# Kernel optimization log

Measured on AMD Instinct MI355X. Metric: run time of the kernel, lower is better.

The kernel has to match this reference:

```python
import jax, jax.numpy as jnp
import numpy as np

CH = (64, 128, 256, 512)
KV = 960
H = 4          # num_attention_heads; each head owns one channel quarter
EPS = 1e-5     # InstanceNorm2d default eps
B, N = 4, 4096

def _qsplit(x):
    # (B,n,c) -> (B,H,n,c//4): contiguous quarter-split along channels (torch .split)
    b, n, c = x.shape
    return x.reshape(b, n, H, c // H).transpose(0, 2, 1, 3)

def _kvsplit(emb_all):
    # quarter j of emb_all = concat over scales of quarter j of each scale's channel block
    b, n, _ = emb_all.shape
    parts, off = [], 0
    for c in CH:
        parts.append(emb_all[:, :, off:off + c].reshape(b, n, H, c // H))
        off += c
    return jnp.concatenate(parts, axis=-1).transpose(0, 2, 1, 3)  # (B,H,n,240)

def _inorm(s):
    # InstanceNorm2d(H), affine=False: normalize each (b,h) map over its (c,k) extent
    m = jnp.mean(s, axis=(2, 3), keepdims=True)
    v = jnp.var(s, axis=(2, 3), keepdims=True)
    return (s - m) * jax.lax.rsqrt(v + EPS)

def _attend(Q, K, V):
    # Q:(B,H,n,cq)  K,V:(B,H,n,240)  -> (B,n,H*cq)  (channel attention: contract over n)
    scores = jnp.einsum('bhnc,bhnk->bhck', Q, K) / np.float32(np.sqrt(KV))
    probs = jax.nn.softmax(_inorm(scores), axis=-1)
    ctx = jnp.einsum('bhck,bhnk->bnhc', probs, V)
    b, n = ctx.shape[:2]
    return ctx.reshape(b, n, -1)

def setup_inputs() -> dict:
    key = jax.random.key(0)
    ks = iter(jax.random.split(key, 48))
    d = {}
    for name, c in [('emb1', 64), ('emb2', 128), ('emb3', 256), ('emb4', 512)]:
        d[name] = jax.random.normal(next(ks), (B, N, c), jnp.float32)
        d[name.replace('emb', 'embd')] = jax.random.normal(next(ks), (B, N, c), jnp.float32)
    d['emb_all'] = jax.random.normal(next(ks), (B, N, KV), jnp.float32)
    d['emb_alld'] = jax.random.normal(next(ks), (B, N, KV), jnp.float32)
    sc = lambda f: float(1.0 / np.sqrt(f))
    for i, c in enumerate(CH):
        c4 = c // H
        d[f'wq{i+1}'] = jax.random.uniform(next(ks), (H, c4, c4), jnp.float32, -sc(c4), sc(c4))
        d[f'wqd{i+1}'] = jax.random.uniform(next(ks), (H, c4, c4), jnp.float32, -sc(c4), sc(c4))
        d[f'wout{i+1}'] = jax.random.uniform(next(ks), (c, c), jnp.float32, -sc(c), sc(c))
        d[f'woutd{i+1}'] = jax.random.uniform(next(ks), (c, c), jnp.float32, -sc(c), sc(c))
    k4 = KV // H
    for nm in ['wk', 'wv', 'wkd', 'wvd']:  # key/value weights are shared across quarters (module uses index [0])
        d[nm] = jax.random.uniform(next(ks), (k4, k4), jnp.float32, -sc(k4), sc(k4))
    return d

def reference(emb1, emb2, emb3, emb4, emb_all, embd1, embd2, embd3, embd4, emb_alld,
              wq1, wq2, wq3, wq4, wqd1, wqd2, wqd3, wqd4,
              wk, wv, wkd, wvd,
              wout1, wout2, wout3, wout4, woutd1, woutd2, woutd3, woutd4):
    Qs = [jnp.einsum('bhnc,hdc->bhnd', _qsplit(e), w) for e, w in
          zip((emb1, emb2, emb3, emb4), (wq1, wq2, wq3, wq4))]
    Qds = [jnp.einsum('bhnc,hdc->bhnd', _qsplit(e), w) for e, w in
           zip((embd1, embd2, embd3, embd4), (wqd1, wqd2, wqd3, wqd4))]
    kvq, kvqd = _kvsplit(emb_all), _kvsplit(emb_alld)
    K  = jnp.einsum('bhnc,dc->bhnd', kvq,  wk)
    V  = jnp.einsum('bhnc,dc->bhnd', kvq,  wv)
    Kd = jnp.einsum('bhnc,dc->bhnd', kvqd, wkd)
    Vd = jnp.einsum('bhnc,dc->bhnd', kvqd, wvd)
    outs = []
    # cross-modal: optical queries attend to DSM K/V and vice versa
    for Q, w in zip(Qs, (wout1, wout2, wout3, wout4)):
        outs.append(jnp.einsum('bnc,dc->bnd', _attend(Q, Kd, Vd), w))
    for Q, w in zip(Qds, (woutd1, woutd2, woutd3, woutd4)):
        outs.append(jnp.einsum('bnc,dc->bnd', _attend(Q, K, V), w))
    return jnp.concatenate(outs, axis=-1)  # (B, N, 2*960)
```

## Files before the change

### kernel.cpp

```cpp
#include <hip/hip_runtime.h>
#include <hip/hip_bf16.h>

typedef __bf16 bf16_t;
typedef __bf16 bf16x8 __attribute__((ext_vector_type(8)));
typedef float f32x4 __attribute__((ext_vector_type(4)));

static constexpr int B_ = 4, N_ = 4096, H_ = 4;
static constexpr int KS = 40;

__device__ __forceinline__ f32x4 mfma_bf16(bf16x8 a, bf16x8 b, f32x4 c) {
  return __builtin_amdgcn_mfma_f32_16x16x32_bf16(a, b, c, 0, 0, 0);
}

__device__ __forceinline__ void stpk4(bf16_t* d, float4 v) {
  bf16_t t[4] = {(bf16_t)v.x, (bf16_t)v.y, (bf16_t)v.z, (bf16_t)v.w};
  *(uint2*)d = *(const uint2*)t;
}
__device__ __forceinline__ void stz8(bf16_t* d) { *(uint2*)d = make_uint2(0u, 0u); }

__device__ __forceinline__ int kvg(int h, int c) {
  if (c < 16)  return h * 16 + c;
  if (c < 48)  return 64 + h * 32 + c - 16;
  if (c < 112) return 192 + h * 64 + c - 48;
  return 448 + h * 128 + c - 112;
}

__device__ __forceinline__ int qsc(int r) { return (r < 16) ? 0 : (r < 48) ? 1 : (r < 112) ? 2 : 3; }

__global__ __launch_bounds__(256) void k_prep_w(
    const float* __restrict__ wk, const float* __restrict__ wv,
    const float* __restrict__ wkd, const float* __restrict__ wvd,
    const float* __restrict__ wo00, const float* __restrict__ wo01,
    const float* __restrict__ wo02, const float* __restrict__ wo03,
    const float* __restrict__ wo10, const float* __restrict__ wo11,
    const float* __restrict__ wo12, const float* __restrict__ wo13,
    bf16_t* __restrict__ Wkvb, bf16_t* __restrict__ Wob) {
  const float* wkv[4] = {wk, wv, wkd, wvd};
  const float* wo[2][4] = {{wo00, wo01, wo02, wo03}, {wo10, wo11, wo12, wo13}};
  const int soff_f4[5] = {0, 1024, 5120, 21504, 87040};
  for (int i = blockIdx.x * 256 + threadIdx.x; i < 231680; i += gridDim.x * 256) {
    if (i < 57600) {
      int t = i / 14400, r = i - t * 14400;
      float4 v = *(const float4*)(wkv[t] + r * 4);
      stpk4(Wkvb + (size_t)t * 57600 + r * 4, v);
    } else {
      int j = i - 57600;
      int mod = j / 87040, jr = j - mod * 87040;
      int s = (jr < 1024) ? 0 : (jr < 5120) ? 1 : (jr < 21504) ? 2 : 3;
      float4 v = *(const float4*)(wo[mod][s] + (jr - soff_f4[s]) * 4);
      stpk4(Wob + (size_t)mod * 348160 + jr * 4, v);
    }
  }
}

__global__ __launch_bounds__(256) void k_kvsplit(
    const float* __restrict__ eA, const float* __restrict__ eB,
    bf16_t* __restrict__ G) {
  const int TOT = 2 * 16 * 4096 * 30;
  for (int i = blockIdx.x * 256 + threadIdx.x; i < TOT; i += gridDim.x * 256) {
    int t = i / 30;
    int cg = i - t * 30;
    int mod = t >> 16;
    int row = t & 65535;
    int bh = row >> 12, n = row & 4095;
    int b = bh >> 2, h = bh & 3;
    int col = kvg(h, cg * 8);
    const float* src = (mod ? eB : eA) + ((size_t)b * N_ + n) * 960 + col;
    float4 v0 = *(const float4*)src;
    float4 v1 = *(const float4*)(src + 4);
    bf16_t o[8] = {(bf16_t)v0.x, (bf16_t)v0.y, (bf16_t)v0.z, (bf16_t)v0.w,
                   (bf16_t)v1.x, (bf16_t)v1.y, (bf16_t)v1.z, (bf16_t)v1.w};
    *(uint4*)(G + (size_t)t * 240 + cg * 8) = *(const uint4*)o;
  }
}

template <int C4>
__global__ __launch_bounds__(256) void k_proj_q(
    const float* __restrict__ e0, const float* __restrict__ w0, bf16_t* __restrict__ o0,
    const float* __restrict__ e1, const float* __restrict__ w1, bf16_t* __restrict__ o1) {
  constexpr int KP = (C4 < 32) ? 32 : C4;
  constexpr int NF = C4 / 16;
  const float* emb = blockIdx.z ? e1 : e0;
  const float* wq = blockIdx.z ? w1 : w0;
  bf16_t* qout = blockIdx.z ? o1 : o0;
  const int h = blockIdx.y;
  const int m0 = blockIdx.x * 128;
  const int b = m0 >> 12, n0 = m0 & 4095;
  const int tid = threadIdx.x, lane = tid & 63, wid = tid >> 6;
  const int l15 = lane & 15, q = lane >> 4;
  __shared__ bf16_t sA[128 * KS];
  __shared__ bf16_t sB[C4 * KS];
  const f32x4 fz = {0.f, 0.f, 0.f, 0.f};
  f32x4 acc[2][NF];
  for (int i = 0; i < 2; i++) for (int f = 0; f < NF; f++) acc[i][f] = fz;
  const float* srow = emb + ((size_t)b * N_ + n0) * (H_ * C4) + h * C4;
  const float* wb = wq + h * C4 * C4;
  for (int k0 = 0; k0 < KP; k0 += 32) {
    __syncthreads();
    for (int idx = tid; idx < 1024; idx += 256) {
      int r = idx >> 3, cg = idx & 7, c = k0 + cg * 4;
      if (c < C4) stpk4(&sA[r * KS + cg * 4], *(const float4*)(srow + (size_t)r * (H_ * C4) + c));
      else stz8(&sA[r * KS + cg * 4]);
    }
    for (int idx = tid; idx < C4 * 8; idx += 256) {
      int dd = idx >> 3, cg = idx & 7, c = k0 + cg * 4;
      if (c < C4) stpk4(&sB[dd * KS + cg * 4], *(const float4*)(wb + dd * C4 + c));
      else stz8(&sB[dd * KS + cg * 4]);
    }
    __syncthreads();
    const bf16_t* ap = &sA[(wid * 32 + l15) * KS + q * 8];
    bf16x8 a0 = *(const bf16x8*)ap;
    bf16x8 a1 = *(const bf16x8*)(ap + 16 * KS);
    for (int f = 0; f < NF; f++) {
      bf16x8 bb = *(const bf16x8*)&sB[(16 * f + l15) * KS + q * 8];
      acc[0][f] = mfma_bf16(a0, bb, acc[0][f]);
      acc[1][f] = mfma_bf16(a1, bb, acc[1][f]);
    }
  }
  bf16_t* qbh = qout + (size_t)(b * H_ + h) * C4 * 4096;
  for (int i = 0; i < 2; i++)
    for (int f = 0; f < NF; f++) {
      bf16_t pk[4];
      for (int r = 0; r < 4; r++) pk[r] = (bf16_t)acc[i][f][r];
      *(uint2*)(qbh + (size_t)(16 * f + l15) * 4096 + n0 + wid * 32 + 16 * i + q * 4) =
          *(const uint2*)pk;
    }
}

__global__ __launch_bounds__(512) void k_proj_kv(
    const bf16_t* __restrict__ G, const bf16_t* __restrict__ Wkvb,
    bf16_t* __restrict__ Kt0, bf16_t* __restrict__ V0,
    bf16_t* __restrict__ Kt1, bf16_t* __restrict__ V1) {
  const int mod = blockIdx.y;
  const bf16_t* src = G + (size_t)mod * ((size_t)B_ * H_ * N_ * 240);
  const bf16_t* wK = Wkvb + (size_t)(2 * mod) * 57600;
  const bf16_t* wV = Wkvb + (size_t)(2 * mod + 1) * 57600;
  bf16_t* Kt = mod ? Kt1 : Kt0;
  bf16_t* V = mod ? V1 : V0;
  const int m0 = blockIdx.x * 128;
  const int bh = m0 >> 12, n0 = m0 & 4095;
  const int tid = threadIdx.x, lane = tid & 63, wid = tid >> 6;
  const int l15 = lane & 15, q = lane >> 4;
  __shared__ bf16_t sA[128 * KS];
  __shared__ bf16_t sB[2][240 * KS];
  const f32x4 fz = {0.f, 0.f, 0.f, 0.f};
  f32x4 accK[15], accV[15];
  for (int f = 0; f < 15; f++) { accK[f] = fz; accV[f] = fz; }
  const bf16_t* arow = src + (size_t)m0 * 240;
  const uint4 z4 = make_uint4(0u, 0u, 0u, 0u);

  const int ar = tid >> 2, ag = tid & 3;
  int bm[4], bd[4], bg[4];
#pragma unroll
  for (int j = 0; j < 4; j++) {
    int idx = tid + 512 * j;
    bm[j] = idx >= 960;
    int jj = idx - (bm[j] ? 960 : 0);
    bd[j] = jj >> 2; bg[j] = jj & 3;
  }
  uint4 ra, rb0, rb1, rb2, rb3;

#define KV_LOAD(K0)                                                                    \
  {                                                                                    \
    int c = (K0) + ag * 8;                                                             \
    ra = (c < 240) ? *(const uint4*)(arow + (size_t)ar * 240 + c) : z4;                \
    int c0_ = (K0) + bg[0] * 8;                                                        \
    rb0 = (c0_ < 240) ? *(const uint4*)((bm[0] ? wV : wK) + bd[0] * 240 + c0_) : z4;   \
    int c1_ = (K0) + bg[1] * 8;                                                        \
    rb1 = (c1_ < 240) ? *(const uint4*)((bm[1] ? wV : wK) + bd[1] * 240 + c1_) : z4;   \
    int c2_ = (K0) + bg[2] * 8;                                                        \
    rb2 = (c2_ < 240) ? *(const uint4*)((bm[2] ? wV : wK) + bd[2] * 240 + c2_) : z4;   \
    if (tid < 384) {                                                                   \
      int c3_ = (K0) + bg[3] * 8;                                                      \
      rb3 = (c3_ < 240) ? *(const uint4*)((bm[3] ? wV : wK) + bd[3] * 240 + c3_) : z4; \
    }                                                                                  \
  }
#define KV_WRITE()                                                                     \
  {                                                                                    \
    *(uint4*)&sA[ar * KS + ag * 8] = ra;                                               \
    *(uint4*)&sB[bm[0]][bd[0] * KS + bg[0] * 8] = rb0;                                 \
    *(uint4*)&sB[bm[1]][bd[1] * KS + bg[1] * 8] = rb1;                                 \
    *(uint4*)&sB[bm[2]][bd[2] * KS + bg[2] * 8] = rb2;                                 \
    if (tid < 384) *(uint4*)&sB[bm[3]][bd[3] * KS + bg[3] * 8] = rb3;                  \
  }

  KV_LOAD(0);
  KV_WRITE();
  for (int t = 0; t < 8; t++) {
    if (t < 7) KV_LOAD((t + 1) * 32);
    __syncthreads();
    bf16x8 a = *(const bf16x8*)&sA[(wid * 16 + l15) * KS + q * 8];
#pragma unroll
    for (int f = 0; f < 15; f++) {
      bf16x8 bk = *(const bf16x8*)&sB[0][(16 * f + l15) * KS + q * 8];
      bf16x8 bv = *(const bf16x8*)&sB[1][(16 * f + l15) * KS + q * 8];
      accK[f] = mfma_bf16(a, bk, accK[f]);
      accV[f] = mfma_bf16(a, bv, accV[f]);
    }
    __syncthreads();
    if (t < 7) KV_WRITE();
  }
#undef KV_LOAD
#undef KV_WRITE

  for (int f = 0; f < 15; f++) {
    bf16_t pk[4];
    for (int r = 0; r < 4; r++) pk[r] = (bf16_t)accK[f][r];
    bf16_t* dst = Kt + ((size_t)bh * 240 + 16 * f + l15) * 4096 + n0 + wid * 16 + q * 4;
    *(uint2*)dst = *(const uint2*)pk;
  }
  bf16_t* orow = V + ((size_t)bh * N_ + n0) * 240;
  for (int f = 0; f < 15; f++)
    for (int r = 0; r < 4; r++) {
      int mm = wid * 16 + q * 4 + r;
      orow[(size_t)mm * 240 + 16 * f + l15] = (bf16_t)accV[f][r];
    }
}

__global__ __launch_bounds__(512) void k_scores_all(
    const bf16_t* __restrict__ Qb, const bf16_t* __restrict__ Kt0,
    const bf16_t* __restrict__ Kt1, float* __restrict__ probs) {
  const size_t KV1 = (size_t)B_ * H_ * N_ * 240;
  const size_t PB1 = (size_t)B_ * H_ * 240 * 240;
  const int qcum[4] = {0, 16, 48, 112};
  const int bh = blockIdx.x;
  const int mod = blockIdx.y >> 4, chunk = blockIdx.y & 15;
  const int ch0 = chunk * 256;
  const bf16_t* ktp = mod ? Kt0 : Kt1;
  const int tid = threadIdx.x, lane = tid & 63, wid = tid >> 6;
  const int l15 = lane & 15, q = lane >> 4;
  __shared__ bf16_t sQ[240 * KS];
  __shared__ bf16_t sK[240 * KS];
  const f32x4 fz = {0.f, 0.f, 0.f, 0.f};
  f32x4 acc[2][15];
  for (int i = 0; i < 2; i++) for (int f = 0; f < 15; f++) acc[i][f] = fz;

  const int row0 = tid >> 2, g8 = (tid & 3) * 8;
  const int row1v = row0 + 128;
  const int row1 = (row1v < 240) ? row1v : 239;
  const bool hasR1 = (tid < 448);
  int s0i = qsc(row0), s1i = qsc(row1);
  const bf16_t* qp0 = Qb + (size_t)mod * KV1 + (size_t)65536 * qcum[s0i] +
                      ((size_t)bh * (16 << s0i) + (row0 - qcum[s0i])) * 4096 + ch0 + g8;
  const bf16_t* qp1 = Qb + (size_t)mod * KV1 + (size_t)65536 * qcum[s1i] +
                      ((size_t)bh * (16 << s1i) + (row1 - qcum[s1i])) * 4096 + ch0 + g8;
  const bf16_t* kp0 = ktp + ((size_t)bh * 240 + row0) * 4096 + ch0 + g8;
  const bf16_t* kp1 = ktp + ((size_t)bh * 240 + row1) * 4096 + ch0 + g8;
  uint4 rq0, rq1, rk0, rk1;

#define SC_LOAD(K0)                                   \
  {                                                   \
    rq0 = *(const uint4*)(qp0 + (K0));                \
    rk0 = *(const uint4*)(kp0 + (K0));                \
    if (hasR1) {                                      \
      rq1 = *(const uint4*)(qp1 + (K0));              \
      rk1 = *(const uint4*)(kp1 + (K0));              \
    }                                                 \
  }
#define SC_WRITE()                                    \
  {                                                   \
    *(uint4*)&sQ[row0 * KS + g8] = rq0;               \
    *(uint4*)&sK[row0 * KS + g8] = rk0;               \
    if (hasR1) {                                      \
      *(uint4*)&sQ[row1v * KS + g8] = rq1;            \
      *(uint4*)&sK[row1v * KS + g8] = rk1;            \
    }                                                 \
  }

  const int cf0 = wid, cf1 = wid + 8;
  SC_LOAD(0);
  SC_WRITE();
  for (int t = 0; t < 8; t++) {
    if (t < 7) SC_LOAD((t + 1) * 32);
    __syncthreads();
    bf16x8 af0 = *(const bf16x8*)&sQ[(16 * cf0 + l15) * KS + q * 8];
    bf16x8 af1;
    if (cf1 < 15) af1 = *(const bf16x8*)&sQ[(16 * cf1 + l15) * KS + q * 8];
#pragma unroll
    for (int f = 0; f < 15; f++) {
      bf16x8 bb = *(const bf16x8*)&sK[(16 * f + l15) * KS + q * 8];
      acc[0][f] = mfma_bf16(af0, bb, acc[0][f]);
      if (cf1 < 15) acc[1][f] = mfma_bf16(af1, bb, acc[1][f]);
    }
    __syncthreads();
    if (t < 7) SC_WRITE();
  }
#undef SC_LOAD
#undef SC_WRITE

  const float rs = 0.0322748612183951f;
  for (int ci = 0; ci < 2; ci++) {
    int cf = wid + 8 * ci;
    if (cf >= 15) continue;
    int cbase = 16 * cf;
    int s = qsc(cbase);
    float* pb = probs + (size_t)mod * PB1 +
                ((size_t)16 * qcum[s] + (size_t)bh * (16 << s)) * 240;
    int crow = cbase - qcum[s] + q * 4;
    for (int f = 0; f < 15; f++)
      for (int r = 0; r < 4; r++)
        atomicAdd(&pb[(size_t)(crow + r) * 240 + 16 * f + l15], acc[ci][f][r] * rs);
  }
}

__global__ __launch_bounds__(256) void k_inorm_softmax(float* __restrict__ p0,
                                                       float* __restrict__ p1, int c4) {
  float* p = (blockIdx.z ? p1 : p0) + (size_t)blockIdx.x * c4 * 240;
  const int tid = threadIdx.x;
  const int tot = c4 * 240;
  float s = 0.f, s2 = 0.f;
  for (int idx = tid; idx < tot; idx += 256) {
    float v = p[idx];
    s += v; s2 += v * v;
  }
#pragma unroll
  for (int off = 32; off > 0; off >>= 1) {
    s += __shfl_xor(s, off);
    s2 += __shfl_xor(s2, off);
  }
  __shared__ float rsum[4], rsum2[4], smv[2];
  const int wid = tid >> 6, lane = tid & 63;
  if (lane == 0) { rsum[wid] = s; rsum2[wid] = s2; }
  __syncthreads();
  if (tid == 0) {
    float ts = rsum[0] + rsum[1] + rsum[2] + rsum[3];
    float ts2 = rsum2[0] + rsum2[1] + rsum2[2] + rsum2[3];
    float mean = ts / tot;
    float var = ts2 / tot - mean * mean;
    smv[0] = mean; smv[1] = rsqrtf(var + 1e-5f);
  }
  __syncthreads();
  const float mean = smv[0], rstd = smv[1];
  for (int c = wid; c < c4; c += 4) {
    float* row = p + (size_t)c * 240;
    float x[4]; float mx = -1e30f;
#pragma unroll
    for (int t = 0; t < 4; t++) {
      int k = lane + 64 * t;
      x[t] = (k < 240) ? (row[k] - mean) * rstd : -1e30f;
      mx = fmaxf(mx, x[t]);
    }
#pragma unroll
    for (int off = 32; off > 0; off >>= 1) mx = fmaxf(mx, __shfl_xor(mx, off));
    float e[4], sum = 0.f;
#pragma unroll
    for (int t = 0; t < 4; t++) {
      int k = lane + 64 * t;
      e[t] = (k < 240) ? expf(x[t] - mx) : 0.f;
      sum += e[t];
    }
#pragma unroll
    for (int off = 32; off > 0; off >>= 1) sum += __shfl_xor(sum, off);
    const float inv = 1.f / sum;
#pragma unroll
    for (int t = 0; t < 4; t++) {
      int k = lane + 64 * t;
      if (k < 240) row[k] = e[t] * inv;
    }
  }
}

template <int C4>
__global__ __launch_bounds__(256) void k_pv(
    const float* __restrict__ p0, const bf16_t* __restrict__ v0, bf16_t* __restrict__ c0p,
    const float* __restrict__ p1, const bf16_t* __restrict__ v1, bf16_t* __restrict__ c1p,
    int chof) {
  constexpr int NF = C4 / 16;
  const float* pr = blockIdx.z ? p1 : p0;
  const bf16_t* v = blockIdx.z ? v1 : v0;
  bf16_t* ctx = blockIdx.z ? c1p : c0p;
  const int bh = blockIdx.y, b = bh >> 2, h = bh & 3;
  const int n0 = blockIdx.x * 128;
  const int tid = threadIdx.x, lane = tid & 63, wid = tid >> 6;
  const int l15 = lane & 15, q = lane >> 4;
  __shared__ bf16_t sV[128 * KS];
  __shared__ bf16_t sP[C4 * KS];
  const f32x4 fz = {0.f, 0.f, 0.f, 0.f};
  f32x4 acc[2][NF];
  for (int i = 0; i < 2; i++) for (int f = 0; f < NF; f++) acc[i][f] = fz;
  const bf16_t* vrow = v + ((size_t)bh * N_ + n0) * 240;
  const float* pb = pr + (size_t)bh * C4 * 240;
  for (int k0 = 0; k0 < 256; k0 += 32) {
    __syncthreads();
    for (int idx = tid; idx < 512; idx += 256) {
      int r = idx >> 2, g = idx & 3, k = k0 + g * 8;
      if (k < 240) *(uint4*)&sV[r * KS + g * 8] = *(const uint4*)(vrow + (size_t)r * 240 + k);
      else *(uint4*)&sV[r * KS + g * 8] = make_uint4(0u, 0u, 0u, 0u);
    }
    for (int idx = tid; idx < C4 * 8; idx += 256) {
      int cc = idx >> 3, cg = idx & 7, k = k0 + cg * 4;
      if (k < 240) stpk4(&sP[cc * KS + cg * 4], *(const float4*)(pb + (size_t)cc * 240 + k));
      else stz8(&sP[cc * KS + cg * 4]);
    }
    __syncthreads();
    const bf16_t* ap = &sV[(wid * 32 + l15) * KS + q * 8];
    bf16x8 a0 = *(const bf16x8*)ap;
    bf16x8 a1 = *(const bf16x8*)(ap + 16 * KS);
    for (int f = 0; f < NF; f++) {
      bf16x8 bb = *(const bf16x8*)&sP[(16 * f + l15) * KS + q * 8];
      acc[0][f] = mfma_bf16(a0, bb, acc[0][f]);
      acc[1][f] = mfma_bf16(a1, bb, acc[1][f]);
    }
  }
  bf16_t* crow = ctx + ((size_t)b * N_ + n0) * 960 + chof + h * C4;
  for (int i = 0; i < 2; i++)
    for (int f = 0; f < NF; f++)
      for (int r = 0; r < 4; r++) {
        int mm = wid * 32 + 16 * i + q * 4 + r;
        crow[(size_t)mm * 960 + 16 * f + l15] = (bf16_t)acc[i][f][r];
      }
}

template <int CS>
__global__ __launch_bounds__(256) void k_wout(
    const bf16_t* __restrict__ c0p, const bf16_t* __restrict__ w0, int ob0,
    const bf16_t* __restrict__ c1p, const bf16_t* __restrict__ w1, int ob1,
    float* __restrict__ out, int chof) {
  constexpr int DT = (CS < 128) ? CS : 128;
  constexpr int NF = DT / 16;
  constexpr int DB = CS / DT;
  const int mod = blockIdx.z / DB, dch = blockIdx.z % DB;
  const bf16_t* ctx = mod ? c1p : c0p;
  const bf16_t* w = mod ? w1 : w0;
  const int obase = (mod ? ob1 : ob0) + dch * DT;
  const int m0 = blockIdx.x * 128;
  const int b = m0 >> 12, n0 = m0 & 4095;
  const int tid = threadIdx.x, lane = tid & 63, wid = tid >> 6;
  const int l15 = lane & 15, q = lane >> 4;
  __shared__ bf16_t sA[128 * KS];
  __shared__ bf16_t sB[DT * KS];
  const f32x4 fz = {0.f, 0.f, 0.f, 0.f};
  f32x4 acc[2][NF];
  for (int i = 0; i < 2; i++) for (int f = 0; f < NF; f++) acc[i][f] = fz;
  const bf16_t* arow = ctx + ((size_t)b * N_ + n0) * 960 + chof;
  const bf16_t* wb = w + (size_t)dch * DT * CS;
  for (int k0 = 0; k0 < CS; k0 += 32) {
    __syncthreads();
    for (int idx = tid; idx < 512; idx += 256) {
      int r = idx >> 2, g = idx & 3, k = k0 + g * 8;
      *(uint4*)&sA[r * KS + g * 8] = *(const uint4*)(arow + (size_t)r * 960 + k);
    }
    for (int idx = tid; idx < DT * 4; idx += 256) {
      int dd = idx >> 2, g = idx & 3, k = k0 + g * 8;
      *(uint4*)&sB[dd * KS + g * 8] = *(const uint4*)(wb + (size_t)dd * CS + k);
    }
    __syncthreads();
    const bf16_t* ap = &sA[(wid * 32 + l15) * KS + q * 8];
    bf16x8 a0 = *(const bf16x8*)ap;
    bf16x8 a1 = *(const bf16x8*)(ap + 16 * KS);
    for (int f = 0; f < NF; f++) {
      bf16x8 bb = *(const bf16x8*)&sB[(16 * f + l15) * KS + q * 8];
      acc[0][f] = mfma_bf16(a0, bb, acc[0][f]);
      acc[1][f] = mfma_bf16(a1, bb, acc[1][f]);
    }
  }
  float* orow = out + ((size_t)b * N_ + n0) * 1920 + obase;
  for (int i = 0; i < 2; i++)
    for (int f = 0; f < NF; f++)
      for (int r = 0; r < 4; r++) {
        int mm = wid * 32 + 16 * i + q * 4 + r;
        orow[(size_t)mm * 1920 + 16 * f + l15] = acc[i][f][r];
      }
}

extern "C" void kernel_launch(void* const* d_in, const int* in_sizes, int n_in,
                              void* d_out, int out_size, void* d_ws, size_t ws_size,
                              hipStream_t stream) {
  (void)in_sizes; (void)n_in; (void)out_size; (void)ws_size;
  const float* emb[2][4];
  const float* wq[2][4];
  const float* wo[2][4];
  for (int s = 0; s < 4; s++) {
    emb[0][s] = (const float*)d_in[2 * s];
    emb[1][s] = (const float*)d_in[2 * s + 1];
    wq[0][s] = (const float*)d_in[10 + 4 * s];
    wq[1][s] = (const float*)d_in[11 + 4 * s];
    wo[0][s] = (const float*)d_in[12 + 4 * s];
    wo[1][s] = (const float*)d_in[13 + 4 * s];
  }
  const float* emb_all = (const float*)d_in[8];
  const float* emb_alld = (const float*)d_in[9];
  const float* wkp = (const float*)d_in[26];
  const float* wvp = (const float*)d_in[27];
  const float* wkdp = (const float*)d_in[28];
  const float* wvdp = (const float*)d_in[29];
  float* out = (float*)d_out;

  bf16_t* w16 = (bf16_t*)d_ws;
  const size_t KV1 = (size_t)B_ * H_ * N_ * 240;
  const size_t PB1 = (size_t)B_ * H_ * 240 * 240;
  bf16_t* Kt0 = w16;
  bf16_t* Kt1 = w16 + KV1;
  bf16_t* V0 = w16 + 2 * KV1;
  bf16_t* V1 = w16 + 3 * KV1;
  bf16_t* Qb = w16 + 4 * KV1;
  float* probs = (float*)(w16 + 6 * KV1);
  bf16_t* Wkvb = (bf16_t*)(probs + 2 * PB1);
  bf16_t* Wob = Wkvb + 230400;
  const int qcum[4] = {0, 16, 48, 112};
  const int chof[4] = {0, 64, 192, 448};
  const int soff[4] = {0, 4096, 20480, 86016};
  const dim3 blk(256);

  k_prep_w<<<dim3(256), blk, 0, stream>>>(wkp, wvp, wkdp, wvdp,
      wo[0][0], wo[0][1], wo[0][2], wo[0][3], wo[1][0], wo[1][1], wo[1][2], wo[1][3],
      Wkvb, Wob);
  hipMemsetAsync(probs, 0, 2 * PB1 * sizeof(float), stream);

  k_kvsplit<<<dim3(2048), blk, 0, stream>>>(emb_all, emb_alld, Qb);
  k_proj_kv<<<dim3(B_ * H_ * N_ / 128, 2), dim3(512), 0, stream>>>(
      Qb, Wkvb, Kt0, V0, Kt1, V1);
  for (int s = 0; s < 4; s++) {
    bf16_t* q0 = Qb + (size_t)B_ * H_ * N_ * qcum[s];
    bf16_t* q1 = q0 + KV1;
    dim3 g(B_ * N_ / 128, H_, 2);
    switch (s) {
      case 0: k_proj_q<16><<<g, blk, 0, stream>>>(emb[0][s], wq[0][s], q0, emb[1][s], wq[1][s], q1); break;
      case 1: k_proj_q<32><<<g, blk, 0, stream>>>(emb[0][s], wq[0][s], q0, emb[1][s], wq[1][s], q1); break;
      case 2: k_proj_q<64><<<g, blk, 0, stream>>>(emb[0][s], wq[0][s], q0, emb[1][s], wq[1][s], q1); break;
      case 3: k_proj_q<128><<<g, blk, 0, stream>>>(emb[0][s], wq[0][s], q0, emb[1][s], wq[1][s], q1); break;
    }
  }
  k_scores_all<<<dim3(B_ * H_, 32), dim3(512), 0, stream>>>(Qb, Kt0, Kt1, probs);
  for (int s = 0; s < 4; s++) {
    float* p0 = probs + (size_t)B_ * H_ * qcum[s] * 240;
    float* p1 = p0 + PB1;
    k_inorm_softmax<<<dim3(B_ * H_, 1, 2), blk, 0, stream>>>(p0, p1, 16 << s);
  }
  for (int s = 0; s < 4; s++) {
    float* p0 = probs + (size_t)B_ * H_ * qcum[s] * 240;
    float* p1 = p0 + PB1;
    bf16_t* cx0 = Qb;
    bf16_t* cx1 = Qb + KV1;
    dim3 g(N_ / 128, B_ * H_, 2);
    switch (s) {
      case 0: k_pv<16><<<g, blk, 0, stream>>>(p0, V1, cx0, p1, V0, cx1, chof[s]); break;
      case 1: k_pv<32><<<g, blk, 0, stream>>>(p0, V1, cx0, p1, V0, cx1, chof[s]); break;
      case 2: k_pv<64><<<g, blk, 0, stream>>>(p0, V1, cx0, p1, V0, cx1, chof[s]); break;
      case 3: k_pv<128><<<g, blk, 0, stream>>>(p0, V1, cx0, p1, V0, cx1, chof[s]); break;
    }
  }
  for (int s = 0; s < 4; s++) {
    const bf16_t* cx0 = Qb;
    const bf16_t* cx1 = Qb + KV1;
    const bf16_t* w0 = Wob + soff[s];
    const bf16_t* w1 = Wob + 348160 + soff[s];
    const int cs = 64 << s;
    const int db = (cs < 128) ? 1 : cs / 128;
    dim3 g(B_ * N_ / 128, 1, 2 * db);
    switch (s) {
      case 0: k_wout<64><<<g, blk, 0, stream>>>(cx0, w0, chof[s], cx1, w1, 960 + chof[s], out, chof[s]); break;
      case 1: k_wout<128><<<g, blk, 0, stream>>>(cx0, w0, chof[s], cx1, w1, 960 + chof[s], out, chof[s]); break;
      case 2: k_wout<256><<<g, blk, 0, stream>>>(cx0, w0, chof[s], cx1, w1, 960 + chof[s], out, chof[s]); break;
      case 3: k_wout<512><<<g, blk, 0, stream>>>(cx0, w0, chof[s], cx1, w1, 960 + chof[s], out, chof[s]); break;
    }
  }
}
```

Before: 912.1 us.

## Fuse per-scale PV kernels into one launch and halve score-kernel split

Replaces the four per-scale k_pv launches with a single k_pv_all kernel. It computes all 240 query channels against each V tile at once, so every V tile is read once instead of once per scale. In a separate change, the scores kernel now covers 512 positions per block instead of 256, which halves the number of blocks and the atomicAdd traffic into probs. In exchange, each PV block uses 512 threads and larger shared memory, and the scores grid becomes smaller, which may reduce parallelism.

```diff
diff --git a/kernel.cpp b/kernel.cpp
--- a/kernel.cpp
+++ b/kernel.cpp
@@ -224,8 +224,8 @@
   const size_t PB1 = (size_t)B_ * H_ * 240 * 240;
   const int qcum[4] = {0, 16, 48, 112};
   const int bh = blockIdx.x;
-  const int mod = blockIdx.y >> 4, chunk = blockIdx.y & 15;
-  const int ch0 = chunk * 256;
+  const int mod = blockIdx.y >> 3, chunk = blockIdx.y & 7;
+  const int ch0 = chunk * 512;
   const bf16_t* ktp = mod ? Kt0 : Kt1;
   const int tid = threadIdx.x, lane = tid & 63, wid = tid >> 6;
   const int l15 = lane & 15, q = lane >> 4;
@@ -270,8 +270,8 @@
   const int cf0 = wid, cf1 = wid + 8;
   SC_LOAD(0);
   SC_WRITE();
-  for (int t = 0; t < 8; t++) {
-    if (t < 7) SC_LOAD((t + 1) * 32);
+  for (int t = 0; t < 16; t++) {
+    if (t < 15) SC_LOAD((t + 1) * 32);
     __syncthreads();
     bf16x8 af0 = *(const bf16x8*)&sQ[(16 * cf0 + l15) * KS + q * 8];
     bf16x8 af1;
@@ -283,7 +283,7 @@
       if (cf1 < 15) acc[1][f] = mfma_bf16(af1, bb, acc[1][f]);
     }
     __syncthreads();
-    if (t < 7) SC_WRITE();
+    if (t < 15) SC_WRITE();
   }
 #undef SC_LOAD
 #undef SC_WRITE
@@ -360,55 +360,60 @@
   }
 }
 
-template <int C4>
-__global__ __launch_bounds__(256) void k_pv(
-    const float* __restrict__ p0, const bf16_t* __restrict__ v0, bf16_t* __restrict__ c0p,
-    const float* __restrict__ p1, const bf16_t* __restrict__ v1, bf16_t* __restrict__ c1p,
-    int chof) {
-  constexpr int NF = C4 / 16;
-  const float* pr = blockIdx.z ? p1 : p0;
-  const bf16_t* v = blockIdx.z ? v1 : v0;
-  bf16_t* ctx = blockIdx.z ? c1p : c0p;
+__global__ __launch_bounds__(512) void k_pv_all(
+    const float* __restrict__ probs, const bf16_t* __restrict__ V0,
+    const bf16_t* __restrict__ V1, bf16_t* __restrict__ ctx0, bf16_t* __restrict__ ctx1) {
+  const size_t PB1 = (size_t)B_ * H_ * 240 * 240;
+  const int qcum[4] = {0, 16, 48, 112};
+  const int chof[4] = {0, 64, 192, 448};
   const int bh = blockIdx.y, b = bh >> 2, h = bh & 3;
+  const int mod = blockIdx.z;
   const int n0 = blockIdx.x * 128;
+  const bf16_t* v = mod ? V0 : V1;
+  bf16_t* ctx = mod ? ctx1 : ctx0;
+  const float* pb_all = probs + (size_t)mod * PB1;
   const int tid = threadIdx.x, lane = tid & 63, wid = tid >> 6;
   const int l15 = lane & 15, q = lane >> 4;
   __shared__ bf16_t sV[128 * KS];
-  __shared__ bf16_t sP[C4 * KS];
+  __shared__ bf16_t sP[240 * KS];
   const f32x4 fz = {0.f, 0.f, 0.f, 0.f};
-  f32x4 acc[2][NF];
-  for (int i = 0; i < 2; i++) for (int f = 0; f < NF; f++) acc[i][f] = fz;
+  f32x4 acc[15];
+  for (int f = 0; f < 15; f++) acc[f] = fz;
   const bf16_t* vrow = v + ((size_t)bh * N_ + n0) * 240;
-  const float* pb = pr + (size_t)bh * C4 * 240;
   for (int k0 = 0; k0 < 256; k0 += 32) {
     __syncthreads();
-    for (int idx = tid; idx < 512; idx += 256) {
-      int r = idx >> 2, g = idx & 3, k = k0 + g * 8;
+    {
+      int r = tid >> 2, g = tid & 3, k = k0 + g * 8;
       if (k < 240) *(uint4*)&sV[r * KS + g * 8] = *(const uint4*)(vrow + (size_t)r * 240 + k);
       else *(uint4*)&sV[r * KS + g * 8] = make_uint4(0u, 0u, 0u, 0u);
     }
-    for (int idx = tid; idx < C4 * 8; idx += 256) {
+    for (int idx = tid; idx < 1920; idx += 512) {
       int cc = idx >> 3, cg = idx & 7, k = k0 + cg * 4;
-      if (k < 240) stpk4(&sP[cc * KS + cg * 4], *(const float4*)(pb + (size_t)cc * 240 + k));
-      else stz8(&sP[cc * KS + cg * 4]);
-    }
-    __syncthreads();
-    const bf16_t* ap = &sV[(wid * 32 + l15) * KS + q * 8];
-    bf16x8 a0 = *(const bf16x8*)ap;
-    bf16x8 a1 = *(const bf16x8*)(ap + 16 * KS);
-    for (int f = 0; f < NF; f++) {
+      if (k < 240) {
+        int s = qsc(cc);
+        const float* prow = pb_all +
+            ((size_t)16 * qcum[s] + (size_t)bh * (16 << s) + (cc - qcum[s])) * 240;
+        stpk4(&sP[cc * KS + cg * 4], *(const float4*)(prow + k));
+      } else {
+        stz8(&sP[cc * KS + cg * 4]);
+      }
+    }
+    __syncthreads();
+    bf16x8 a = *(const bf16x8*)&sV[(wid * 16 + l15) * KS + q * 8];
+#pragma unroll
+    for (int f = 0; f < 15; f++) {
       bf16x8 bb = *(const bf16x8*)&sP[(16 * f + l15) * KS + q * 8];
-      acc[0][f] = mfma_bf16(a0, bb, acc[0][f]);
-      acc[1][f] = mfma_bf16(a1, bb, acc[1][f]);
-    }
-  }
-  bf16_t* crow = ctx + ((size_t)b * N_ + n0) * 960 + chof + h * C4;
-  for (int i = 0; i < 2; i++)
-    for (int f = 0; f < NF; f++)
-      for (int r = 0; r < 4; r++) {
-        int mm = wid * 32 + 16 * i + q * 4 + r;
-        crow[(size_t)mm * 960 + 16 * f + l15] = (bf16_t)acc[i][f][r];
-      }
+      acc[f] = mfma_bf16(a, bb, acc[f]);
+    }
+  }
+  for (int f = 0; f < 15; f++) {
+    int s = qsc(16 * f);
+    int colbase = chof[s] + h * (16 << s) + 16 * f - qcum[s];
+    for (int r = 0; r < 4; r++) {
+      int mm = 16 * wid + q * 4 + r;
+      ctx[((size_t)b * N_ + n0 + mm) * 960 + colbase + l15] = (bf16_t)acc[f][r];
+    }
+  }
 }
 
 template <int CS>
@@ -521,25 +526,14 @@
       case 3: k_proj_q<128><<<g, blk, 0, stream>>>(emb[0][s], wq[0][s], q0, emb[1][s], wq[1][s], q1); break;
     }
   }
-  k_scores_all<<<dim3(B_ * H_, 32), dim3(512), 0, stream>>>(Qb, Kt0, Kt1, probs);
+  k_scores_all<<<dim3(B_ * H_, 16), dim3(512), 0, stream>>>(Qb, Kt0, Kt1, probs);
   for (int s = 0; s < 4; s++) {
     float* p0 = probs + (size_t)B_ * H_ * qcum[s] * 240;
     float* p1 = p0 + PB1;
     k_inorm_softmax<<<dim3(B_ * H_, 1, 2), blk, 0, stream>>>(p0, p1, 16 << s);
   }
-  for (int s = 0; s < 4; s++) {
-    float* p0 = probs + (size_t)B_ * H_ * qcum[s] * 240;
-    float* p1 = p0 + PB1;
-    bf16_t* cx0 = Qb;
-    bf16_t* cx1 = Qb + KV1;
-    dim3 g(N_ / 128, B_ * H_, 2);
-    switch (s) {
-      case 0: k_pv<16><<<g, blk, 0, stream>>>(p0, V1, cx0, p1, V0, cx1, chof[s]); break;
-      case 1: k_pv<32><<<g, blk, 0, stream>>>(p0, V1, cx0, p1, V0, cx1, chof[s]); break;
-      case 2: k_pv<64><<<g, blk, 0, stream>>>(p0, V1, cx0, p1, V0, cx1, chof[s]); break;
-      case 3: k_pv<128><<<g, blk, 0, stream>>>(p0, V1, cx0, p1, V0, cx1, chof[s]); break;
-    }
-  }
+  k_pv_all<<<dim3(N_ / 128, B_ * H_, 2), dim3(512), 0, stream>>>(
+      probs, V0, V1, Qb, Qb + KV1);
   for (int s = 0; s < 4; s++) {
     const bf16_t* cx0 = Qb;
     const bf16_t* cx1 = Qb + KV1;
```

Result: faster. 826.6 us (-9.4%).
